# Performance work log

Measured on AMD Instinct MI355X. Metric: run time of the kernel, lower is better.

Reference implementation:

```python
import jax, jax.numpy as jnp
import numpy as np

N = 50000
E = 800000
IN, HID, OUT = 128, 128, 64


def setup_inputs() -> dict:
    key = jax.random.key(0)
    ks = jax.random.split(key, 12)
    x = jax.random.normal(ks[0], (N, IN), dtype=jnp.float32)
    src = jax.random.randint(ks[1], (E,), 0, N)
    dst = jax.random.randint(ks[2], (E,), 0, N)
    edge_index = jnp.stack([src, dst]).astype(jnp.int64)
    def lin(k, fan_in, fan_out):
        s = 1.0 / np.sqrt(fan_in)
        return jax.random.uniform(k, (fan_in, fan_out), jnp.float32, -s, s)
    return {
        "x": x,
        "edge_index": edge_index,
        "w_l0": lin(ks[3], IN, HID), "b0": jnp.zeros((HID,), jnp.float32), "w_r0": lin(ks[4], IN, HID),
        "w_l1": lin(ks[5], HID, HID), "b1": jnp.zeros((HID,), jnp.float32), "w_r1": lin(ks[6], HID, HID),
        "w_l2": lin(ks[7], HID, OUT), "b2": jnp.zeros((OUT,), jnp.float32), "w_r2": lin(ks[8], HID, OUT),
    }


def _sage_conv(x, src, dst, w_l, b, w_r, num_nodes):
    # mean aggregation of source features onto destination nodes
    msg = x[src]                                            # [E, d]
    summed = jax.ops.segment_sum(msg, dst, num_segments=num_nodes)  # [N, d]
    deg = jax.ops.segment_sum(jnp.ones((src.shape[0],), x.dtype), dst, num_segments=num_nodes)
    aggr = summed / jnp.maximum(deg, 1.0)[:, None]
    # out = lin_l(aggr) + lin_r(x_root); bias only on lin_l (PyG SAGEConv default)
    return aggr @ w_l + b + x @ w_r


def reference(x, edge_index, w_l0, b0, w_r0, w_l1, b1, w_r1, w_l2, b2, w_r2):
    src, dst = edge_index[0].astype(jnp.int32), edge_index[1].astype(jnp.int32)
    n = x.shape[0]
    h = jax.nn.relu(_sage_conv(x, src, dst, w_l0, b0, w_r0, n))  # dropout: eval mode -> identity
    h = jax.nn.relu(_sage_conv(h, src, dst, w_l1, b1, w_r1, n))
    return _sage_conv(h, src, dst, w_l2, b2, w_r2, n)
```

## Files before the change

### kernel.cpp

```cpp
#include <hip/hip_runtime.h>
#include <cstdint>
#include <cstddef>


#define HID 128
#define NSLICE 8
#define FILL_BLOCKS_PER_SLICE 256
#define CAP 64
#define CNT_STRIDE 32

using short8 = __attribute__((ext_vector_type(8))) short;
using f32x4  = __attribute__((ext_vector_type(4))) float;


__device__ __forceinline__ unsigned short f32_to_bf16(float f)
{
    union { float f; unsigned int i; } c; c.f = f;
    const unsigned int x = c.i;
    const unsigned int r = x + 0x7fffu + ((x >> 16) & 1u);
    return (unsigned short)(r >> 16);
}

__device__ __forceinline__ float bf16_hi_to_f32(unsigned int hi16_in_low)
{
    union { unsigned int i; float f; } c; c.i = hi16_in_low << 16;
    return c.f;
}


#define PREP_THREADS (2 * 2 * HID * HID + 2 * 64 * HID)

__global__ __launch_bounds__(256) void prep_wt_zero_kernel(
    const float* __restrict__ wl0, const float* __restrict__ wr0,
    const float* __restrict__ wl1, const float* __restrict__ wr1,
    const float* __restrict__ wl2, const float* __restrict__ wr2,
    unsigned short* __restrict__ wt0, unsigned short* __restrict__ wt1,
    unsigned short* __restrict__ wt2, int* __restrict__ cnt, int n)
{
    const int idx = blockIdx.x * 256 + threadIdx.x;
    const int per128 = 2 * HID * HID;
    if (idx < per128) {
        const int k = idx & (HID - 1), c = idx >> 7;
        const float v = (c < HID) ? wl0[(size_t)k * HID + c] : wr0[(size_t)k * HID + (c - HID)];
        wt0[idx] = f32_to_bf16(v);
    } else if (idx < 2 * per128) {
        const int j = idx - per128;
        const int k = j & (HID - 1), c = j >> 7;
        const float v = (c < HID) ? wl1[(size_t)k * HID + c] : wr1[(size_t)k * HID + (c - HID)];
        wt1[j] = f32_to_bf16(v);
    } else if (idx < PREP_THREADS) {
        const int j = idx - 2 * per128;
        const int k = j & (HID - 1), c = j >> 7;
        const float v = (c < 64) ? wl2[(size_t)k * 64 + c] : wr2[(size_t)k * 64 + (c - 64)];
        wt2[j] = f32_to_bf16(v);
    } else {
        const int j = idx - PREP_THREADS;
        if (j < n) cnt[(size_t)j * CNT_STRIDE] = 0;
    }
}


__global__ __launch_bounds__(256) void bucket_fill_sliced_kernel(
    const int* __restrict__ src, const int* __restrict__ dst,
    int* __restrict__ cnt, int* __restrict__ esrc, int E, int n)
{
    const int slice = blockIdx.x & (NSLICE - 1);
    const int nps   = (n + NSLICE - 1) / NSLICE;
    const int lo    = slice * nps;
    const int hi    = min(lo + nps, n);
    const int stride = FILL_BLOCKS_PER_SLICE * 256;
    int e = (blockIdx.x >> 3) * 256 + threadIdx.x;
    for (; e < E; e += stride) {
        const int d = dst[e];
        if (d >= lo && d < hi) {
            const int s = src[e];
            if ((unsigned)s < (unsigned)n) {
                const int p = atomicAdd(&cnt[(size_t)d * CNT_STRIDE], 1);
                if (p < CAP) esrc[(size_t)d * CAP + p] = s;
            }
        }
    }
}


template <int DOUT, bool IN_F32, bool R_BF16>
__global__ __launch_bounds__(256) void sage_mfma_gemm(
    const void* __restrict__ hin,
    const unsigned short* __restrict__ wtc,
    const float* __restrict__ bias,
    unsigned short* __restrict__ p, void* __restrict__ r, int n)
{
    constexpr int TOTC = 2 * DOUT;
    constexpr int CPW  = TOTC / 64;

    const int tx   = threadIdx.x;
    const int wv   = tx >> 6;
    const int lane = tx & 63;
    const int quad = lane >> 4;
    const int l15  = lane & 15;

    short8 B[CPW][4];
#pragma unroll
    for (int t = 0; t < CPW; ++t) {
        const int c = (wv * CPW + t) * 16 + l15;
#pragma unroll
        for (int q = 0; q < 4; ++q)
            B[t][q] = *(const short8*)(wtc + (size_t)c * HID + q * 32 + quad * 8);
    }

    const int slabs = (n + 15) >> 4;
    for (int slab = blockIdx.x; slab < slabs; slab += gridDim.x) {
        const int r0 = slab * 16;
        const int rr = min(r0 + l15, n - 1);

        short8 A[4];
        if (IN_F32) {
            const float* hf = (const float*)hin;
#pragma unroll
            for (int q = 0; q < 4; ++q) {
                const float4 f0 = *(const float4*)(hf + (size_t)rr * HID + q * 32 + quad * 8);
                const float4 f1 = *(const float4*)(hf + (size_t)rr * HID + q * 32 + quad * 8 + 4);
                short8 a;
                a[0] = (short)f32_to_bf16(f0.x); a[1] = (short)f32_to_bf16(f0.y);
                a[2] = (short)f32_to_bf16(f0.z); a[3] = (short)f32_to_bf16(f0.w);
                a[4] = (short)f32_to_bf16(f1.x); a[5] = (short)f32_to_bf16(f1.y);
                a[6] = (short)f32_to_bf16(f1.z); a[7] = (short)f32_to_bf16(f1.w);
                A[q] = a;
            }
        } else {
            const unsigned short* hb = (const unsigned short*)hin;
#pragma unroll
            for (int q = 0; q < 4; ++q)
                A[q] = *(const short8*)(hb + (size_t)rr * HID + q * 32 + quad * 8);
        }

        f32x4 acc[CPW];
#pragma unroll
        for (int t = 0; t < CPW; ++t) acc[t] = (f32x4){0.f, 0.f, 0.f, 0.f};
#pragma unroll
        for (int q = 0; q < 4; ++q)
#pragma unroll
            for (int t = 0; t < CPW; ++t)
                acc[t] = __builtin_amdgcn_mfma_f32_16x16x32_bf16(A[q], B[t][q], acc[t], 0, 0, 0);

#pragma unroll
        for (int t = 0; t < CPW; ++t) {
            const int c0  = (wv * CPW + t) * 16;
            const int col = c0 + l15;
            if (c0 < DOUT) {
#pragma unroll
                for (int i = 0; i < 4; ++i) {
                    const int row = r0 + quad * 4 + i;
                    if (row < n) p[(size_t)row * DOUT + col] = f32_to_bf16(acc[t][i]);
                }
            } else {
                const float bv = bias[col - DOUT];
#pragma unroll
                for (int i = 0; i < 4; ++i) {
                    const int row = r0 + quad * 4 + i;
                    if (row < n) {
                        const float v = acc[t][i] + bv;
                        if (R_BF16)
                            ((unsigned short*)r)[(size_t)row * DOUT + (col - DOUT)] = f32_to_bf16(v);
                        else
                            ((float*)r)[(size_t)row * DOUT + (col - DOUT)] = v;
                    }
                }
            }
        }
    }
}


template <int DOUT, bool RELU, bool OUTBF16, bool R_BF16>
__global__ __launch_bounds__(256) void sage_post_aggregate(
    const unsigned short* __restrict__ p, const void* __restrict__ r,
    const int* __restrict__ cnt, const int* __restrict__ esrc,
    void* __restrict__ out, int n)
{
    const int wid  = threadIdx.x >> 6;
    const int lane = threadIdx.x & 63;
    const int node = blockIdx.x * 4 + wid;
    if (node >= n) return;
    const int dg   = cnt[(size_t)node * CNT_STRIDE];
    const int degc = min(dg, CAP);
    const float inv = 1.0f / fmaxf((float)dg, 1.0f);

    const int sidx = esrc[(size_t)node * CAP + lane];

    if constexpr (DOUT == 128) {
        float ax[8], ay[8];
#pragma unroll
        for (int j = 0; j < 8; ++j) { ax[j] = 0.f; ay[j] = 0.f; }
        for (int e0 = 0; e0 < degc; e0 += 8) {
#pragma unroll
            for (int j = 0; j < 8; ++j) {
                const int slot = e0 + j;
                const float w  = (slot < degc) ? 1.0f : 0.0f;
                const int s    = __shfl(sidx, min(slot, degc - 1), 64);
                const unsigned int v = *(const unsigned int*)(&p[(size_t)s * DOUT + lane * 2]);
                ax[j] = fmaf(w, bf16_hi_to_f32(v & 0xffffu), ax[j]);
                ay[j] = fmaf(w, bf16_hi_to_f32(v >> 16), ay[j]);
            }
        }
        float sx = ((ax[0] + ax[1]) + (ax[2] + ax[3])) + ((ax[4] + ax[5]) + (ax[6] + ax[7]));
        float sy = ((ay[0] + ay[1]) + (ay[2] + ay[3])) + ((ay[4] + ay[5]) + (ay[6] + ay[7]));
        float rx, ry;
        if (R_BF16) {
            const unsigned int rv = ((const unsigned int*)r)[(size_t)node * (DOUT / 2) + lane];
            rx = bf16_hi_to_f32(rv & 0xffffu);
            ry = bf16_hi_to_f32(rv >> 16);
        } else {
            const float2 rv = *((const float2*)((const float*)r + (size_t)node * DOUT) + lane);
            rx = rv.x; ry = rv.y;
        }
        float ox = sx * inv + rx;
        float oy = sy * inv + ry;
        if (RELU) { ox = fmaxf(ox, 0.f); oy = fmaxf(oy, 0.f); }
        if (OUTBF16) {
            const unsigned int pk = ((unsigned int)f32_to_bf16(oy) << 16) | (unsigned int)f32_to_bf16(ox);
            ((unsigned int*)out)[(size_t)node * (DOUT / 2) + lane] = pk;
        } else {
            float2 o; o.x = ox; o.y = oy;
            *((float2*)((float*)out + (size_t)node * DOUT) + lane) = o;
        }
    } else {
        float a[8];
#pragma unroll
        for (int j = 0; j < 8; ++j) a[j] = 0.f;
        for (int e0 = 0; e0 < degc; e0 += 8) {
#pragma unroll
            for (int j = 0; j < 8; ++j) {
                const int slot = e0 + j;
                const float w  = (slot < degc) ? 1.0f : 0.0f;
                const int s    = __shfl(sidx, min(slot, degc - 1), 64);
                const unsigned short u = p[(size_t)s * DOUT + lane];
                a[j] = fmaf(w, bf16_hi_to_f32((unsigned int)u), a[j]);
            }
        }
        float sa = ((a[0] + a[1]) + (a[2] + a[3])) + ((a[4] + a[5]) + (a[6] + a[7]));
        float rv;
        if (R_BF16) {
            const unsigned short u = ((const unsigned short*)r)[(size_t)node * DOUT + lane];
            rv = bf16_hi_to_f32((unsigned int)u);
        } else {
            rv = ((const float*)r)[(size_t)node * DOUT + lane];
        }
        float o = sa * inv + rv;
        if (RELU) o = fmaxf(o, 0.f);
        ((float*)out)[(size_t)node * DOUT + lane] = o;
    }
}


static inline size_t align_up(size_t v, size_t a) { return (v + a - 1) & ~(a - 1); }

extern "C" void kernel_launch(void* const* d_in, const int* in_sizes, int n_in,
                              void* d_out, int out_size, void* d_ws, size_t ws_size,
                              hipStream_t stream)
{
    const float* x   = (const float*)d_in[0];
    const int*   ei  = (const int*)d_in[1];
    const float* wl0 = (const float*)d_in[2];
    const float* b0  = (const float*)d_in[3];
    const float* wr0 = (const float*)d_in[4];
    const float* wl1 = (const float*)d_in[5];
    const float* b1  = (const float*)d_in[6];
    const float* wr1 = (const float*)d_in[7];
    const float* wl2 = (const float*)d_in[8];
    const float* b2  = (const float*)d_in[9];
    const float* wr2 = (const float*)d_in[10];
    float*       out = (float*)d_out;

    const int N = in_sizes[0] / HID;
    const int E = in_sizes[1] / 2;
    const int* src = ei;
    const int* dst = ei + E;

    char*  ws  = (char*)d_ws;
    size_t off = 0;
    int* cnt      = (int*)(ws + off); off = align_up(off + (size_t)N * CNT_STRIDE * 4, 256);
    int* esrc     = (int*)(ws + off); off = align_up(off + (size_t)N * CAP * 4, 256);
    unsigned short* pbuf = (unsigned short*)(ws + off); off = align_up(off + (size_t)N * HID * 2, 256);
    unsigned short* rb16 = (unsigned short*)(ws + off); off = align_up(off + (size_t)N * HID * 2, 256);
    float* rbf32  = (float*)(ws + off); off = align_up(off + (size_t)N * HID * 4, 256);
    unsigned short* hbf = (unsigned short*)(ws + off); off = align_up(off + (size_t)N * HID * 2, 256);
    unsigned short* wt0 = (unsigned short*)(ws + off); off = align_up(off + (size_t)2 * HID * HID * 2, 256);
    unsigned short* wt1 = (unsigned short*)(ws + off); off = align_up(off + (size_t)2 * HID * HID * 2, 256);
    unsigned short* wt2 = (unsigned short*)(ws + off); off = align_up(off + (size_t)HID * HID * 2, 256);
    (void)ws_size; (void)n_in; (void)out_size;

    prep_wt_zero_kernel<<<(PREP_THREADS + N + 255) / 256, 256, 0, stream>>>(
        wl0, wr0, wl1, wr1, wl2, wr2, wt0, wt1, wt2, cnt, N);

    bucket_fill_sliced_kernel<<<NSLICE * FILL_BLOCKS_PER_SLICE, 256, 0, stream>>>(
        src, dst, cnt, esrc, E, N);

    const int aggGrid  = (N + 3) / 4;
    const int gemmGrid = 1024;

    sage_mfma_gemm<128, true, true><<<gemmGrid, 256, 0, stream>>>(x, wt0, b0, pbuf, rb16, N);
    sage_post_aggregate<128, true, true, true><<<aggGrid, 256, 0, stream>>>(pbuf, rb16, cnt, esrc, hbf, N);

    sage_mfma_gemm<128, false, true><<<gemmGrid, 256, 0, stream>>>(hbf, wt1, b1, pbuf, rb16, N);
    sage_post_aggregate<128, true, true, true><<<aggGrid, 256, 0, stream>>>(pbuf, rb16, cnt, esrc, hbf, N);

    sage_mfma_gemm<64, false, false><<<gemmGrid, 256, 0, stream>>>(hbf, wt2, b2, pbuf, rbf32, N);
    sage_post_aggregate<64, false, false, false><<<aggGrid, 256, 0, stream>>>(pbuf, rbf32, cnt, esrc, out, N);
}
```

Before: 283.4 us.

## Fuse bucket fill with layer-0 GEMM and vectorize gather with 16-byte row loads

Merges the edge bucket-fill kernel and the first-layer MFMA GEMM into one launch, with blocks split by index between the two independent tasks so they overlap and one launch is removed. The aggregation kernel is restructured so each lane loads 8 bf16 values (16 bytes) per neighbor and several neighbors are processed in parallel across lane groups, followed by a cross-group shuffle reduction. Only one lane group then writes the outputs with vector stores. This cuts the number of memory instructions per gathered row but adds shuffle reductions and leaves most lanes idle during the epilogue.

```diff
diff --git a/kernel.cpp b/kernel.cpp
--- a/kernel.cpp
+++ b/kernel.cpp
@@ -6,6 +6,8 @@
 #define HID 128
 #define NSLICE 8
 #define FILL_BLOCKS_PER_SLICE 256
+#define FILL_BLOCKS (NSLICE * FILL_BLOCKS_PER_SLICE)
+#define GEMM_BLOCKS 1024
 #define CAP 64
 #define CNT_STRIDE 32
 
@@ -25,6 +27,11 @@
 {
     union { unsigned int i; float f; } c; c.i = hi16_in_low << 16;
     return c.f;
+}
+
+__device__ __forceinline__ unsigned int pack_bf16(float a, float b)
+{
+    return ((unsigned int)f32_to_bf16(b) << 16) | (unsigned int)f32_to_bf16(a);
 }
 
 
@@ -60,16 +67,16 @@
 }
 
 
-__global__ __launch_bounds__(256) void bucket_fill_sliced_kernel(
-    const int* __restrict__ src, const int* __restrict__ dst,
+__device__ __forceinline__ void fill_body(
+    int bid, const int* __restrict__ src, const int* __restrict__ dst,
     int* __restrict__ cnt, int* __restrict__ esrc, int E, int n)
 {
-    const int slice = blockIdx.x & (NSLICE - 1);
+    const int slice = bid & (NSLICE - 1);
     const int nps   = (n + NSLICE - 1) / NSLICE;
     const int lo    = slice * nps;
     const int hi    = min(lo + nps, n);
     const int stride = FILL_BLOCKS_PER_SLICE * 256;
-    int e = (blockIdx.x >> 3) * 256 + threadIdx.x;
+    int e = (bid >> 3) * 256 + threadIdx.x;
     for (; e < E; e += stride) {
         const int d = dst[e];
         if (d >= lo && d < hi) {
@@ -84,14 +91,13 @@
 
 
 template <int DOUT, bool IN_F32, bool R_BF16>
-__global__ __launch_bounds__(256) void sage_mfma_gemm(
-    const void* __restrict__ hin,
-    const unsigned short* __restrict__ wtc,
+__device__ __forceinline__ void gemm_body(
+    int bid, int nblk,
+    const void* __restrict__ hin, const unsigned short* __restrict__ wtc,
     const float* __restrict__ bias,
     unsigned short* __restrict__ p, void* __restrict__ r, int n)
 {
-    constexpr int TOTC = 2 * DOUT;
-    constexpr int CPW  = TOTC / 64;
+    constexpr int CPW = (2 * DOUT) / 64;
 
     const int tx   = threadIdx.x;
     const int wv   = tx >> 6;
@@ -109,7 +115,7 @@
     }
 
     const int slabs = (n + 15) >> 4;
-    for (int slab = blockIdx.x; slab < slabs; slab += gridDim.x) {
+    for (int slab = bid; slab < slabs; slab += nblk) {
         const int r0 = slab * 16;
         const int rr = min(r0 + l15, n - 1);
 
@@ -171,6 +177,29 @@
     }
 }
 
+template <int DOUT, bool IN_F32, bool R_BF16>
+__global__ __launch_bounds__(256) void sage_mfma_gemm(
+    const void* __restrict__ hin, const unsigned short* __restrict__ wtc,
+    const float* __restrict__ bias,
+    unsigned short* __restrict__ p, void* __restrict__ r, int n)
+{
+    gemm_body<DOUT, IN_F32, R_BF16>(blockIdx.x, gridDim.x, hin, wtc, bias, p, r, n);
+}
+
+
+__global__ __launch_bounds__(256) void fill_gemm0_fused_kernel(
+    const int* __restrict__ src, const int* __restrict__ dst,
+    int* __restrict__ cnt, int* __restrict__ esrc, int E,
+    const void* __restrict__ x, const unsigned short* __restrict__ wt0,
+    const float* __restrict__ b0,
+    unsigned short* __restrict__ p, void* __restrict__ r, int n)
+{
+    if (blockIdx.x < FILL_BLOCKS)
+        fill_body(blockIdx.x, src, dst, cnt, esrc, E, n);
+    else
+        gemm_body<128, true, true>(blockIdx.x - FILL_BLOCKS, GEMM_BLOCKS, x, wt0, b0, p, r, n);
+}
+
 
 template <int DOUT, bool RELU, bool OUTBF16, bool R_BF16>
 __global__ __launch_bounds__(256) void sage_post_aggregate(
@@ -189,66 +218,126 @@
     const int sidx = esrc[(size_t)node * CAP + lane];
 
     if constexpr (DOUT == 128) {
-        float ax[8], ay[8];
-#pragma unroll
-        for (int j = 0; j < 8; ++j) { ax[j] = 0.f; ay[j] = 0.f; }
-        for (int e0 = 0; e0 < degc; e0 += 8) {
-#pragma unroll
-            for (int j = 0; j < 8; ++j) {
-                const int slot = e0 + j;
+        const int g  = lane >> 4;
+        const int lo = lane & 15;
+        float acc[4][8];
+#pragma unroll
+        for (int j = 0; j < 4; ++j)
+#pragma unroll
+            for (int c = 0; c < 8; ++c) acc[j][c] = 0.f;
+
+        for (int e0 = 0; e0 < degc; e0 += 16) {
+#pragma unroll
+            for (int j = 0; j < 4; ++j) {
+                const int slot = e0 + j * 4 + g;
                 const float w  = (slot < degc) ? 1.0f : 0.0f;
                 const int s    = __shfl(sidx, min(slot, degc - 1), 64);
-                const unsigned int v = *(const unsigned int*)(&p[(size_t)s * DOUT + lane * 2]);
-                ax[j] = fmaf(w, bf16_hi_to_f32(v & 0xffffu), ax[j]);
-                ay[j] = fmaf(w, bf16_hi_to_f32(v >> 16), ay[j]);
-            }
-        }
-        float sx = ((ax[0] + ax[1]) + (ax[2] + ax[3])) + ((ax[4] + ax[5]) + (ax[6] + ax[7]));
-        float sy = ((ay[0] + ay[1]) + (ay[2] + ay[3])) + ((ay[4] + ay[5]) + (ay[6] + ay[7]));
-        float rx, ry;
-        if (R_BF16) {
-            const unsigned int rv = ((const unsigned int*)r)[(size_t)node * (DOUT / 2) + lane];
-            rx = bf16_hi_to_f32(rv & 0xffffu);
-            ry = bf16_hi_to_f32(rv >> 16);
-        } else {
-            const float2 rv = *((const float2*)((const float*)r + (size_t)node * DOUT) + lane);
-            rx = rv.x; ry = rv.y;
-        }
-        float ox = sx * inv + rx;
-        float oy = sy * inv + ry;
-        if (RELU) { ox = fmaxf(ox, 0.f); oy = fmaxf(oy, 0.f); }
-        if (OUTBF16) {
-            const unsigned int pk = ((unsigned int)f32_to_bf16(oy) << 16) | (unsigned int)f32_to_bf16(ox);
-            ((unsigned int*)out)[(size_t)node * (DOUT / 2) + lane] = pk;
-        } else {
-            float2 o; o.x = ox; o.y = oy;
-            *((float2*)((float*)out + (size_t)node * DOUT) + lane) = o;
+                const short8 v = *(const short8*)(p + (size_t)s * DOUT + lo * 8);
+#pragma unroll
+                for (int c = 0; c < 8; ++c)
+                    acc[j][c] = fmaf(w, bf16_hi_to_f32((unsigned short)v[c]), acc[j][c]);
+            }
+        }
+        float s8[8];
+#pragma unroll
+        for (int c = 0; c < 8; ++c) {
+            float t = (acc[0][c] + acc[1][c]) + (acc[2][c] + acc[3][c]);
+            t += __shfl_xor(t, 16, 64);
+            t += __shfl_xor(t, 32, 64);
+            s8[c] = t * inv;
+        }
+        if (g == 0) {
+            float rc[8];
+            if (R_BF16) {
+                const short8 rv = *(const short8*)((const unsigned short*)r + (size_t)node * DOUT + lo * 8);
+#pragma unroll
+                for (int c = 0; c < 8; ++c) rc[c] = bf16_hi_to_f32((unsigned short)rv[c]);
+            } else {
+                const float4 r0 = *(const float4*)((const float*)r + (size_t)node * DOUT + lo * 8);
+                const float4 r1 = *(const float4*)((const float*)r + (size_t)node * DOUT + lo * 8 + 4);
+                rc[0] = r0.x; rc[1] = r0.y; rc[2] = r0.z; rc[3] = r0.w;
+                rc[4] = r1.x; rc[5] = r1.y; rc[6] = r1.z; rc[7] = r1.w;
+            }
+            float o[8];
+#pragma unroll
+            for (int c = 0; c < 8; ++c) {
+                o[c] = s8[c] + rc[c];
+                if (RELU) o[c] = fmaxf(o[c], 0.f);
+            }
+            if (OUTBF16) {
+                uint4 st;
+                st.x = pack_bf16(o[0], o[1]); st.y = pack_bf16(o[2], o[3]);
+                st.z = pack_bf16(o[4], o[5]); st.w = pack_bf16(o[6], o[7]);
+                *(uint4*)((unsigned short*)out + (size_t)node * DOUT + lo * 8) = st;
+            } else {
+                float4 s0, s1;
+                s0.x = o[0]; s0.y = o[1]; s0.z = o[2]; s0.w = o[3];
+                s1.x = o[4]; s1.y = o[5]; s1.z = o[6]; s1.w = o[7];
+                *(float4*)((float*)out + (size_t)node * DOUT + lo * 8) = s0;
+                *(float4*)((float*)out + (size_t)node * DOUT + lo * 8 + 4) = s1;
+            }
         }
     } else {
-        float a[8];
-#pragma unroll
-        for (int j = 0; j < 8; ++j) a[j] = 0.f;
-        for (int e0 = 0; e0 < degc; e0 += 8) {
-#pragma unroll
-            for (int j = 0; j < 8; ++j) {
-                const int slot = e0 + j;
+        const int g  = lane >> 3;
+        const int lo = lane & 7;
+        float acc[2][8];
+#pragma unroll
+        for (int j = 0; j < 2; ++j)
+#pragma unroll
+            for (int c = 0; c < 8; ++c) acc[j][c] = 0.f;
+
+        for (int e0 = 0; e0 < degc; e0 += 16) {
+#pragma unroll
+            for (int j = 0; j < 2; ++j) {
+                const int slot = e0 + j * 8 + g;
                 const float w  = (slot < degc) ? 1.0f : 0.0f;
                 const int s    = __shfl(sidx, min(slot, degc - 1), 64);
-                const unsigned short u = p[(size_t)s * DOUT + lane];
-                a[j] = fmaf(w, bf16_hi_to_f32((unsigned int)u), a[j]);
-            }
-        }
-        float sa = ((a[0] + a[1]) + (a[2] + a[3])) + ((a[4] + a[5]) + (a[6] + a[7]));
-        float rv;
-        if (R_BF16) {
-            const unsigned short u = ((const unsigned short*)r)[(size_t)node * DOUT + lane];
-            rv = bf16_hi_to_f32((unsigned int)u);
-        } else {
-            rv = ((const float*)r)[(size_t)node * DOUT + lane];
-        }
-        float o = sa * inv + rv;
-        if (RELU) o = fmaxf(o, 0.f);
-        ((float*)out)[(size_t)node * DOUT + lane] = o;
+                const short8 v = *(const short8*)(p + (size_t)s * DOUT + lo * 8);
+#pragma unroll
+                for (int c = 0; c < 8; ++c)
+                    acc[j][c] = fmaf(w, bf16_hi_to_f32((unsigned short)v[c]), acc[j][c]);
+            }
+        }
+        float s8[8];
+#pragma unroll
+        for (int c = 0; c < 8; ++c) {
+            float t = acc[0][c] + acc[1][c];
+            t += __shfl_xor(t, 8, 64);
+            t += __shfl_xor(t, 16, 64);
+            t += __shfl_xor(t, 32, 64);
+            s8[c] = t * inv;
+        }
+        if (g == 0) {
+            float rc[8];
+            if (R_BF16) {
+                const short8 rv = *(const short8*)((const unsigned short*)r + (size_t)node * DOUT + lo * 8);
+#pragma unroll
+                for (int c = 0; c < 8; ++c) rc[c] = bf16_hi_to_f32((unsigned short)rv[c]);
+            } else {
+                const float4 r0 = *(const float4*)((const float*)r + (size_t)node * DOUT + lo * 8);
+                const float4 r1 = *(const float4*)((const float*)r + (size_t)node * DOUT + lo * 8 + 4);
+                rc[0] = r0.x; rc[1] = r0.y; rc[2] = r0.z; rc[3] = r0.w;
+                rc[4] = r1.x; rc[5] = r1.y; rc[6] = r1.z; rc[7] = r1.w;
+            }
+            float o[8];
+#pragma unroll
+            for (int c = 0; c < 8; ++c) {
+                o[c] = s8[c] + rc[c];
+                if (RELU) o[c] = fmaxf(o[c], 0.f);
+            }
+            if (OUTBF16) {
+                uint4 st;
+                st.x = pack_bf16(o[0], o[1]); st.y = pack_bf16(o[2], o[3]);
+                st.z = pack_bf16(o[4], o[5]); st.w = pack_bf16(o[6], o[7]);
+                *(uint4*)((unsigned short*)out + (size_t)node * DOUT + lo * 8) = st;
+            } else {
+                float4 s0, s1;
+                s0.x = o[0]; s0.y = o[1]; s0.z = o[2]; s0.w = o[3];
+                s1.x = o[4]; s1.y = o[5]; s1.z = o[6]; s1.w = o[7];
+                *(float4*)((float*)out + (size_t)node * DOUT + lo * 8) = s0;
+                *(float4*)((float*)out + (size_t)node * DOUT + lo * 8 + 4) = s1;
+            }
+        }
     }
 }
 
@@ -293,18 +382,16 @@
     prep_wt_zero_kernel<<<(PREP_THREADS + N + 255) / 256, 256, 0, stream>>>(
         wl0, wr0, wl1, wr1, wl2, wr2, wt0, wt1, wt2, cnt, N);
 
-    bucket_fill_sliced_kernel<<<NSLICE * FILL_BLOCKS_PER_SLICE, 256, 0, stream>>>(
-        src, dst, cnt, esrc, E, N);
-
-    const int aggGrid  = (N + 3) / 4;
-    const int gemmGrid = 1024;
-
-    sage_mfma_gemm<128, true, true><<<gemmGrid, 256, 0, stream>>>(x, wt0, b0, pbuf, rb16, N);
+    const int aggGrid = (N + 3) / 4;
+
+    fill_gemm0_fused_kernel<<<FILL_BLOCKS + GEMM_BLOCKS, 256, 0, stream>>>(
+        src, dst, cnt, esrc, E, x, wt0, b0, pbuf, rb16, N);
+
     sage_post_aggregate<128, true, true, true><<<aggGrid, 256, 0, stream>>>(pbuf, rb16, cnt, esrc, hbf, N);
 
-    sage_mfma_gemm<128, false, true><<<gemmGrid, 256, 0, stream>>>(hbf, wt1, b1, pbuf, rb16, N);
+    sage_mfma_gemm<128, false, true><<<GEMM_BLOCKS, 256, 0, stream>>>(hbf, wt1, b1, pbuf, rb16, N);
     sage_post_aggregate<128, true, true, true><<<aggGrid, 256, 0, stream>>>(pbuf, rb16, cnt, esrc, hbf, N);
 
-    sage_mfma_gemm<64, false, false><<<gemmGrid, 256, 0, stream>>>(hbf, wt2, b2, pbuf, rbf32, N);
+    sage_mfma_gemm<64, false, false><<<GEMM_BLOCKS, 256, 0, stream>>>(hbf, wt2, b2, pbuf, rbf32, N);
     sage_post_aggregate<64, false, false, false><<<aggGrid, 256, 0, stream>>>(pbuf, rbf32, cnt, esrc, out, N);
 }
```

Result: slower. 300.1 us (+5.9%).
